# Optimization experiments

Hardware: AMD Instinct MI355X
Metric: run time of the kernel (lower is better)

Reference implementation:

```python
import jax, jax.numpy as jnp
import numpy as np


def setup_inputs() -> dict:
    key = jax.random.key(0)
    kq, kk, kv, km = jax.random.split(key, 4)
    B, H, S, D = 2, 16, 2048, 64
    Q = jax.random.normal(kq, (B, H, S, D), dtype=jnp.float32)
    K = jax.random.normal(kk, (B, H, S, D), dtype=jnp.float32)
    V = jax.random.normal(kv, (B, H, S, D), dtype=jnp.float32)
    mask = jax.random.randint(km, (B, 1, S, S), 0, 2).astype(jnp.bool_)
    return {"Q": Q, "K": K, "V": V, "mask": mask}


def reference(Q, K, V, mask):
    # scores: [B, H, Sq, Sk]
    scores = jnp.einsum("bhqd,bhkd->bhqk", Q, K)
    neg = jnp.finfo(scores.dtype).min
    # Faithful to original: mask fill happens BEFORE the sqrt(d) scaling.
    scores = jnp.where(mask, neg, scores)
    inv_sqrt_d = 1.0 / jnp.sqrt(jnp.asarray(Q.shape[-1], dtype=scores.dtype))
    attn = jax.nn.softmax(scores * inv_sqrt_d, axis=-1)
    return jnp.einsum("bhqk,bhkd->bhqd", attn, V)
```

## Files before the change

### kernel.cpp

```cpp
#include <hip/hip_runtime.h>
#include <stdint.h>


#define SQ 2048
#define DH 64

using bf16x8  = __attribute__((ext_vector_type(8)))  __bf16;
using f32x4   = __attribute__((ext_vector_type(4)))  float;
using ushort8 = __attribute__((ext_vector_type(8)))  unsigned short;
using ushort4v= __attribute__((ext_vector_type(4)))  unsigned short;

static __device__ __forceinline__ unsigned short f2bf(float f) {
    union { float f; uint32_t u; } c; c.f = f;
    return (unsigned short)((c.u + 0x8000u) >> 16);
}

static __device__ __forceinline__ uint32_t pkbf(float a, float b) {
    union { __bf16 h[2]; uint32_t u; } t;
    t.h[0] = (__bf16)a; t.h[1] = (__bf16)b;
    return t.u;
}

static __device__ __forceinline__ f32x4 mfma16(bf16x8 a, bf16x8 b, f32x4 c) {
    return __builtin_amdgcn_mfma_f32_16x16x32_bf16(a, b, c, 0, 0, 0);
}

static __device__ __forceinline__ void gload16(const void* g, void* l) {
    __builtin_amdgcn_global_load_lds(
        (const __attribute__((address_space(1))) void*)g,
        (__attribute__((address_space(3))) void*)l, 16, 0, 0);
}

__global__ __launch_bounds__(256)
void prep_kernel(const int* __restrict__ mask, const float* __restrict__ K,
                 const float* __restrict__ V, unsigned long long* __restrict__ words,
                 unsigned short* __restrict__ Kb, unsigned short* __restrict__ Vt) {
    __shared__ unsigned short tl[64][66];
    const int bx  = blockIdx.x;
    const int tid = threadIdx.x;
    if (bx < 32768) {
        int gid = bx * 256 + tid;
        int mv = mask[gid];
        unsigned long long b = __ballot(mv != 0);
        if ((gid & 63) == 0) words[gid >> 6] = b;
    } else if (bx < 36864) {
        int gid = (bx - 32768) * 256 + tid;
        float4 v = ((const float4*)K)[gid];
        ushort4v t;
        t[0]=f2bf(v.x); t[1]=f2bf(v.y); t[2]=f2bf(v.z); t[3]=f2bf(v.w);
        ((ushort4v*)Kb)[gid] = t;
    } else {
        const int vbx = bx - 36864;
        const int kt  = vbx & 31;
        const size_t bh = vbx >> 5;
        const float* vp = V + (bh * SQ + (size_t)kt * 64) * DH;
        #pragma unroll
        for (int i = 0; i < 4; ++i) {
            int idx = tid + 256 * i;
            int key = idx >> 4;
            int dc  = (idx & 15) * 4;
            float4 v = *(const float4*)(vp + (size_t)key * DH + dc);
            tl[key][dc + 0] = f2bf(v.x);
            tl[key][dc + 1] = f2bf(v.y);
            tl[key][dc + 2] = f2bf(v.z);
            tl[key][dc + 3] = f2bf(v.w);
        }
        __syncthreads();
        unsigned short* op = Vt + bh * DH * SQ + (size_t)kt * 64;
        #pragma unroll
        for (int i = 0; i < 4; ++i) {
            int idx = tid + 256 * i;
            int d  = idx >> 4;
            int kc = (idx & 15) * 4;
            ushort4v t;
            t[0] = tl[kc + 0][d]; t[1] = tl[kc + 1][d];
            t[2] = tl[kc + 2][d]; t[3] = tl[kc + 3][d];
            *(ushort4v*)(op + (size_t)d * SQ + kc) = t;
        }
    }
}

__global__ __launch_bounds__(128, 2)
void attn_kernel(const float* __restrict__ Q,
                 const unsigned short* __restrict__ Kb,
                 const unsigned short* __restrict__ Vtg,
                 const unsigned long long* __restrict__ Mw,
                 float* __restrict__ out) {
    __shared__ __align__(16) unsigned short Ks[2][64 * 64];
    __shared__ __align__(16) unsigned short Vs[2][64 * 64];
    __shared__ __align__(16) unsigned short Ps[2 * 16 * 64];

    const int tid  = threadIdx.x;
    const int w    = tid >> 6;
    const int l    = tid & 63;
    const int quad = l >> 4;
    const int c16  = l & 15;
    const int bx = blockIdx.x;
    const int hh = bx & 15;
    const int b  = (bx >> 4) & 1;
    const int qt = bx >> 5;

    const size_t bh = (size_t)b * 16 + hh;
    const float* Qp = Q + bh * SQ * DH;
    const int qw = qt * 64 + 32 * w;

    const unsigned long long* Mrow0 = Mw + ((size_t)b * SQ + qw + c16) * (SQ / 64);
    const unsigned long long* Mrow1 = Mrow0 + 16 * (SQ / 64);

    const int lr = l >> 3;
    const int gg = l & 7;
    const int off16 = ((gg ^ lr) << 4);
    const char* Kg = (const char*)(Kb  + bh * (size_t)SQ * DH);
    const char* Vg = (const char*)(Vtg + bh * (size_t)DH * SQ);
    const char* kS[4]; const char* vS[4];
    #pragma unroll
    for (int i = 0; i < 4; ++i) {
        int row = 32 * w + 8 * i + lr;
        kS[i] = Kg + (size_t)row * 128  + off16;
        vS[i] = Vg + (size_t)row * 4096 + off16;
    }

    bf16x8 qf[2][2];
    #pragma unroll
    for (int sub = 0; sub < 2; ++sub) {
        const float* qr = Qp + (size_t)(qw + 16 * sub + c16) * DH;
        #pragma unroll
        for (int c = 0; c < 2; ++c) {
            int d0 = 32 * c + 8 * quad;
            float4 a  = *(const float4*)(qr + d0);
            float4 b4 = *(const float4*)(qr + d0 + 4);
            ushort8 t;
            t[0]=f2bf(a.x);  t[1]=f2bf(a.y);  t[2]=f2bf(a.z);  t[3]=f2bf(a.w);
            t[4]=f2bf(b4.x); t[5]=f2bf(b4.y); t[6]=f2bf(b4.z); t[7]=f2bf(b4.w);
            qf[sub][c] = __builtin_bit_cast(bf16x8, t);
        }
    }

    f32x4 o0[4], o1[4];
    float lsum0 = 0.f, lsum1 = 0.f;
    #pragma unroll
    for (int i = 0; i < 4; ++i) { o0[i] = (f32x4)(0.f); o1[i] = (f32x4)(0.f); }

    unsigned short* Pw = Ps + w * (16 * 64);
    const int xg = (c16 & 7);
    int gfrag[2];
    #pragma unroll
    for (int c = 0; c < 2; ++c) gfrag[c] = ((4 * c + quad) ^ xg) << 3;
    int poff[4];
    #pragma unroll
    for (int nb = 0; nb < 4; ++nb)
        poff[nb] = c16 * 64 + (((2 * nb + (quad >> 1)) ^ xg) << 3) + 4 * (quad & 1);
    const int paoff0 = c16 * 64 + gfrag[0];
    const int paoff1 = c16 * 64 + gfrag[1];

    unsigned long long mw0 = Mrow0[0], mw1 = Mrow1[0];
    #pragma unroll
    for (int i = 0; i < 4; ++i) {
        gload16(kS[i], &Ks[0][(4 * w + i) * 512]);
        gload16(vS[i], &Vs[0][(4 * w + i) * 512]);
        kS[i] += 8192; vS[i] += 128;
    }
    __syncthreads();

    for (int t = 0; t < 32; ++t) {
        const int cur = t & 1;

        unsigned long long nmw0 = 0, nmw1 = 0;
        if (t < 31) {
            #pragma unroll
            for (int i = 0; i < 4; ++i) {
                gload16(kS[i], &Ks[cur ^ 1][(4 * w + i) * 512]);
                gload16(vS[i], &Vs[cur ^ 1][(4 * w + i) * 512]);
                kS[i] += 8192; vS[i] += 128;
            }
            nmw0 = Mrow0[t + 1];
            nmw1 = Mrow1[t + 1];
        }

        const unsigned short* Kc = Ks[cur];
        const unsigned short* Vc = Vs[cur];

        f32x4 s0[4], s1[4];
        #pragma unroll
        for (int i = 0; i < 4; ++i) { s0[i] = (f32x4)(0.f); s1[i] = (f32x4)(0.f); }
        __builtin_amdgcn_s_setprio(1);
        #pragma unroll
        for (int c = 0; c < 2; ++c) {
            #pragma unroll
            for (int nb = 0; nb < 4; ++nb) {
                bf16x8 kb = __builtin_bit_cast(bf16x8,
                    *(const ushort8*)&Kc[(c16 + 16 * nb) * 64 + gfrag[c]]);
                s0[nb] = mfma16(kb, qf[0][c], s0[nb]);
                s1[nb] = mfma16(kb, qf[1][c], s1[nb]);
            }
        }
        __builtin_amdgcn_s_setprio(0);

        uint32_t pk0[4][2], pk1[4][2];
        {
            const unsigned long long sh = mw0 >> (4 * quad);
            #pragma unroll
            for (int nb = 0; nb < 4; ++nb) {
                float pv[4];
                #pragma unroll
                for (int r = 0; r < 4; ++r) {
                    float e = __builtin_amdgcn_exp2f(fmaf(s0[nb][r], 0.18033688f, -5.7707802f));
                    pv[r] = ((sh >> (16 * nb + r)) & 1ull) ? 0.0f : e;
                    lsum0 += pv[r];
                }
                pk0[nb][0] = pkbf(pv[0], pv[1]);
                pk0[nb][1] = pkbf(pv[2], pv[3]);
            }
            #pragma unroll
            for (int nb = 0; nb < 4; ++nb) {
                uint2 wv; wv.x = pk0[nb][0]; wv.y = pk0[nb][1];
                *(uint2*)&Pw[poff[nb]] = wv;
            }
        }
        {
            const unsigned long long sh = mw1 >> (4 * quad);
            #pragma unroll
            for (int nb = 0; nb < 4; ++nb) {
                float pv[4];
                #pragma unroll
                for (int r = 0; r < 4; ++r) {
                    float e = __builtin_amdgcn_exp2f(fmaf(s1[nb][r], 0.18033688f, -5.7707802f));
                    pv[r] = ((sh >> (16 * nb + r)) & 1ull) ? 0.0f : e;
                    lsum1 += pv[r];
                }
                pk1[nb][0] = pkbf(pv[0], pv[1]);
                pk1[nb][1] = pkbf(pv[2], pv[3]);
            }
        }
        bf16x8 pa0[2], pa1[2];
        pa0[0] = __builtin_bit_cast(bf16x8, *(const ushort8*)&Pw[paoff0]);
        pa0[1] = __builtin_bit_cast(bf16x8, *(const ushort8*)&Pw[paoff1]);
        #pragma unroll
        for (int nb = 0; nb < 4; ++nb) {
            uint2 wv; wv.x = pk1[nb][0]; wv.y = pk1[nb][1];
            *(uint2*)&Pw[poff[nb]] = wv;
        }
        pa1[0] = __builtin_bit_cast(bf16x8, *(const ushort8*)&Pw[paoff0]);
        pa1[1] = __builtin_bit_cast(bf16x8, *(const ushort8*)&Pw[paoff1]);

        __builtin_amdgcn_s_setprio(1);
        #pragma unroll
        for (int c = 0; c < 2; ++c) {
            #pragma unroll
            for (int db = 0; db < 4; ++db) {
                bf16x8 vb = __builtin_bit_cast(bf16x8,
                    *(const ushort8*)&Vc[(c16 + 16 * db) * 64 + gfrag[c]]);
                o0[db] = mfma16(vb, pa0[c], o0[db]);
                o1[db] = mfma16(vb, pa1[c], o1[db]);
            }
        }
        __builtin_amdgcn_s_setprio(0);

        __syncthreads();
        mw0 = nmw0; mw1 = nmw1;
    }

    {
        float v = lsum0;
        v += __shfl_xor(v, 16, 64);
        v += __shfl_xor(v, 32, 64);
        const float rinv = 1.0f / v;
        float* op = out + (bh * SQ + (size_t)(qw + c16)) * DH + 4 * quad;
        #pragma unroll
        for (int db = 0; db < 4; ++db) {
            float4 st;
            st.x = o0[db][0] * rinv; st.y = o0[db][1] * rinv;
            st.z = o0[db][2] * rinv; st.w = o0[db][3] * rinv;
            *(float4*)(op + 16 * db) = st;
        }
    }
    {
        float v = lsum1;
        v += __shfl_xor(v, 16, 64);
        v += __shfl_xor(v, 32, 64);
        const float rinv = 1.0f / v;
        float* op = out + (bh * SQ + (size_t)(qw + 16 + c16)) * DH + 4 * quad;
        #pragma unroll
        for (int db = 0; db < 4; ++db) {
            float4 st;
            st.x = o1[db][0] * rinv; st.y = o1[db][1] * rinv;
            st.z = o1[db][2] * rinv; st.w = o1[db][3] * rinv;
            *(float4*)(op + 16 * db) = st;
        }
    }
}

extern "C" void kernel_launch(void* const* d_in, const int* in_sizes, int n_in,
                              void* d_out, int out_size, void* d_ws, size_t ws_size,
                              hipStream_t stream) {
    const float* Q    = (const float*)d_in[0];
    const float* K    = (const float*)d_in[1];
    const float* V    = (const float*)d_in[2];
    const int*   mask = (const int*)d_in[3];
    float* out = (float*)d_out;

    char* ws = (char*)d_ws;
    unsigned long long* mwords = (unsigned long long*)ws;
    unsigned short* Kb = (unsigned short*)(ws + (1 << 20));
    unsigned short* Vt = (unsigned short*)(ws + (1 << 20) + (8 << 20));

    prep_kernel<<<dim3(37888), dim3(256), 0, stream>>>(mask, K, V, mwords, Kb, Vt);
    attn_kernel<<<dim3(1024), dim3(128), 0, stream>>>(Q, Kb, Vt, mwords, out);
}
```

Baseline: 190.8 us.

## Load K/V fragments straight from global into registers, one wave per block

Removes the shared-memory K/V double buffering and block-wide barriers. Each 64-thread block handles 32 query rows and reads its K and V MFMA fragments directly from global memory into registers, prefetching the next K tile in software. This cuts LDS traffic and synchronisation, but drops the sharing of K/V tiles between waves, so global/L2 traffic grows. It also raises register pressure from holding the fragments.

```diff
diff --git a/kernel.cpp b/kernel.cpp
--- a/kernel.cpp
+++ b/kernel.cpp
@@ -23,12 +23,6 @@
 
 static __device__ __forceinline__ f32x4 mfma16(bf16x8 a, bf16x8 b, f32x4 c) {
     return __builtin_amdgcn_mfma_f32_16x16x32_bf16(a, b, c, 0, 0, 0);
-}
-
-static __device__ __forceinline__ void gload16(const void* g, void* l) {
-    __builtin_amdgcn_global_load_lds(
-        (const __attribute__((address_space(1))) void*)g,
-        (__attribute__((address_space(3))) void*)l, 16, 0, 0);
 }
 
 __global__ __launch_bounds__(256)
@@ -80,45 +74,42 @@
     }
 }
 
-__global__ __launch_bounds__(128, 2)
+#define LOADKB(dst, kt)                                                          \
+    {                                                                            \
+        _Pragma("unroll")                                                        \
+        for (int nb = 0; nb < 4; ++nb) {                                         \
+            _Pragma("unroll")                                                    \
+            for (int c = 0; c < 2; ++c)                                          \
+                dst[nb][c] = __builtin_bit_cast(bf16x8, *(const ushort8*)        \
+                    (kRow + (size_t)(kt) * 8192 + nb * 2048 + c * 64));          \
+        }                                                                        \
+    }
+
+__global__ __launch_bounds__(64)
 void attn_kernel(const float* __restrict__ Q,
                  const unsigned short* __restrict__ Kb,
                  const unsigned short* __restrict__ Vtg,
                  const unsigned long long* __restrict__ Mw,
                  float* __restrict__ out) {
-    __shared__ __align__(16) unsigned short Ks[2][64 * 64];
-    __shared__ __align__(16) unsigned short Vs[2][64 * 64];
-    __shared__ __align__(16) unsigned short Ps[2 * 16 * 64];
-
-    const int tid  = threadIdx.x;
-    const int w    = tid >> 6;
-    const int l    = tid & 63;
+    __shared__ __align__(16) unsigned short Ps[16 * 64];
+
+    const int l    = threadIdx.x;
     const int quad = l >> 4;
     const int c16  = l & 15;
     const int bx = blockIdx.x;
     const int hh = bx & 15;
     const int b  = (bx >> 4) & 1;
-    const int qt = bx >> 5;
+    const int qs = bx >> 5;
 
     const size_t bh = (size_t)b * 16 + hh;
     const float* Qp = Q + bh * SQ * DH;
-    const int qw = qt * 64 + 32 * w;
+    const int qw = qs * 32;
 
     const unsigned long long* Mrow0 = Mw + ((size_t)b * SQ + qw + c16) * (SQ / 64);
     const unsigned long long* Mrow1 = Mrow0 + 16 * (SQ / 64);
 
-    const int lr = l >> 3;
-    const int gg = l & 7;
-    const int off16 = ((gg ^ lr) << 4);
-    const char* Kg = (const char*)(Kb  + bh * (size_t)SQ * DH);
-    const char* Vg = (const char*)(Vtg + bh * (size_t)DH * SQ);
-    const char* kS[4]; const char* vS[4];
-    #pragma unroll
-    for (int i = 0; i < 4; ++i) {
-        int row = 32 * w + 8 * i + lr;
-        kS[i] = Kg + (size_t)row * 128  + off16;
-        vS[i] = Vg + (size_t)row * 4096 + off16;
-    }
+    const char* kRow = (const char*)(Kb  + bh * (size_t)SQ * DH) + c16 * 128  + quad * 16;
+    const char* vRow = (const char*)(Vtg + bh * (size_t)DH * SQ) + c16 * 4096 + quad * 16;
 
     bf16x8 qf[2][2];
     #pragma unroll
@@ -141,7 +132,7 @@
     #pragma unroll
     for (int i = 0; i < 4; ++i) { o0[i] = (f32x4)(0.f); o1[i] = (f32x4)(0.f); }
 
-    unsigned short* Pw = Ps + w * (16 * 64);
+    unsigned short* Pw = Ps;
     const int xg = (c16 & 7);
     int gfrag[2];
     #pragma unroll
@@ -153,32 +144,17 @@
     const int paoff0 = c16 * 64 + gfrag[0];
     const int paoff1 = c16 * 64 + gfrag[1];
 
-    unsigned long long mw0 = Mrow0[0], mw1 = Mrow1[0];
-    #pragma unroll
-    for (int i = 0; i < 4; ++i) {
-        gload16(kS[i], &Ks[0][(4 * w + i) * 512]);
-        gload16(vS[i], &Vs[0][(4 * w + i) * 512]);
-        kS[i] += 8192; vS[i] += 128;
-    }
-    __syncthreads();
-
-    for (int t = 0; t < 32; ++t) {
-        const int cur = t & 1;
-
-        unsigned long long nmw0 = 0, nmw1 = 0;
-        if (t < 31) {
-            #pragma unroll
-            for (int i = 0; i < 4; ++i) {
-                gload16(kS[i], &Ks[cur ^ 1][(4 * w + i) * 512]);
-                gload16(vS[i], &Vs[cur ^ 1][(4 * w + i) * 512]);
-                kS[i] += 8192; vS[i] += 128;
-            }
-            nmw0 = Mrow0[t + 1];
-            nmw1 = Mrow1[t + 1];
-        }
-
-        const unsigned short* Kc = Ks[cur];
-        const unsigned short* Vc = Vs[cur];
+    auto tile = [&](int kt, bf16x8 (&kb)[4][2]) {
+        unsigned long long mw0 = Mrow0[kt], mw1 = Mrow1[kt];
+
+        bf16x8 vb[4][2];
+        #pragma unroll
+        for (int db = 0; db < 4; ++db) {
+            #pragma unroll
+            for (int c = 0; c < 2; ++c)
+                vb[db][c] = __builtin_bit_cast(bf16x8, *(const ushort8*)
+                    (vRow + db * 65536 + (size_t)kt * 128 + c * 64));
+        }
 
         f32x4 s0[4], s1[4];
         #pragma unroll
@@ -188,10 +164,8 @@
         for (int c = 0; c < 2; ++c) {
             #pragma unroll
             for (int nb = 0; nb < 4; ++nb) {
-                bf16x8 kb = __builtin_bit_cast(bf16x8,
-                    *(const ushort8*)&Kc[(c16 + 16 * nb) * 64 + gfrag[c]]);
-                s0[nb] = mfma16(kb, qf[0][c], s0[nb]);
-                s1[nb] = mfma16(kb, qf[1][c], s1[nb]);
+                s0[nb] = mfma16(kb[nb][c], qf[0][c], s0[nb]);
+                s1[nb] = mfma16(kb[nb][c], qf[1][c], s1[nb]);
             }
         }
         __builtin_amdgcn_s_setprio(0);
@@ -248,16 +222,20 @@
         for (int c = 0; c < 2; ++c) {
             #pragma unroll
             for (int db = 0; db < 4; ++db) {
-                bf16x8 vb = __builtin_bit_cast(bf16x8,
-                    *(const ushort8*)&Vc[(c16 + 16 * db) * 64 + gfrag[c]]);
-                o0[db] = mfma16(vb, pa0[c], o0[db]);
-                o1[db] = mfma16(vb, pa1[c], o1[db]);
+                o0[db] = mfma16(vb[db][c], pa0[c], o0[db]);
+                o1[db] = mfma16(vb[db][c], pa1[c], o1[db]);
             }
         }
         __builtin_amdgcn_s_setprio(0);
-
-        __syncthreads();
-        mw0 = nmw0; mw1 = nmw1;
+    };
+
+    bf16x8 kbA[4][2], kbB[4][2];
+    LOADKB(kbA, 0);
+    for (int tt = 0; tt < 32; tt += 2) {
+        LOADKB(kbB, tt + 1);
+        tile(tt, kbA);
+        if (tt + 2 < 32) LOADKB(kbA, tt + 2);
+        tile(tt + 1, kbB);
     }
 
     {
@@ -305,5 +283,5 @@
     unsigned short* Vt = (unsigned short*)(ws + (1 << 20) + (8 << 20));
 
     prep_kernel<<<dim3(37888), dim3(256), 0, stream>>>(mask, K, V, mwords, Kb, Vt);
-    attn_kernel<<<dim3(1024), dim3(128), 0, stream>>>(Q, Kb, Vt, mwords, out);
-}
+    attn_kernel<<<dim3(2048), dim3(64), 0, stream>>>(Q, Kb, Vt, mwords, out);
+}
```

Result: slower. 250.8 us (+31.5%).

## Load V fragments directly into registers and hand-pipeline K staging with waitcnt

Applied to the files above, without the earlier changes.

V tiles are no longer staged through shared memory. Each lane reads its MFMA B-operand fragments straight from global memory into registers, double-buffered across two tiles. The K loop is unrolled by two with explicit vmcnt and lgkmcnt waits, sched barriers and s_barrier calls, so prefetch of the next tiles overlaps compute. This cuts LDS traffic and footprint, which may allow more occupancy, but it adds register pressure and less-coalesced global V reads, and the hand-counted vmcnt values are fragile.

```diff
diff --git a/kernel.cpp b/kernel.cpp
--- a/kernel.cpp
+++ b/kernel.cpp
@@ -87,7 +87,6 @@
                  const unsigned long long* __restrict__ Mw,
                  float* __restrict__ out) {
     __shared__ __align__(16) unsigned short Ks[2][64 * 64];
-    __shared__ __align__(16) unsigned short Vs[2][64 * 64];
     __shared__ __align__(16) unsigned short Ps[2 * 16 * 64];
 
     const int tid  = threadIdx.x;
@@ -111,14 +110,12 @@
     const int gg = l & 7;
     const int off16 = ((gg ^ lr) << 4);
     const char* Kg = (const char*)(Kb  + bh * (size_t)SQ * DH);
-    const char* Vg = (const char*)(Vtg + bh * (size_t)DH * SQ);
-    const char* kS[4]; const char* vS[4];
-    #pragma unroll
-    for (int i = 0; i < 4; ++i) {
-        int row = 32 * w + 8 * i + lr;
-        kS[i] = Kg + (size_t)row * 128  + off16;
-        vS[i] = Vg + (size_t)row * 4096 + off16;
-    }
+    const char* kBase[4];
+    #pragma unroll
+    for (int i = 0; i < 4; ++i)
+        kBase[i] = Kg + (size_t)(32 * w + 8 * i + lr) * 128 + off16;
+
+    const char* vRow = (const char*)(Vtg + bh * (size_t)DH * SQ) + c16 * 4096 + quad * 16;
 
     bf16x8 qf[2][2];
     #pragma unroll
@@ -153,33 +150,22 @@
     const int paoff0 = c16 * 64 + gfrag[0];
     const int paoff1 = c16 * 64 + gfrag[1];
 
-    unsigned long long mw0 = Mrow0[0], mw1 = Mrow1[0];
-    #pragma unroll
-    for (int i = 0; i < 4; ++i) {
-        gload16(kS[i], &Ks[0][(4 * w + i) * 512]);
-        gload16(vS[i], &Vs[0][(4 * w + i) * 512]);
-        kS[i] += 8192; vS[i] += 128;
-    }
-    __syncthreads();
-
-    for (int t = 0; t < 32; ++t) {
-        const int cur = t & 1;
-
-        unsigned long long nmw0 = 0, nmw1 = 0;
-        if (t < 31) {
-            #pragma unroll
-            for (int i = 0; i < 4; ++i) {
-                gload16(kS[i], &Ks[cur ^ 1][(4 * w + i) * 512]);
-                gload16(vS[i], &Vs[cur ^ 1][(4 * w + i) * 512]);
-                kS[i] += 8192; vS[i] += 128;
-            }
-            nmw0 = Mrow0[t + 1];
-            nmw1 = Mrow1[t + 1];
-        }
-
-        const unsigned short* Kc = Ks[cur];
-        const unsigned short* Vc = Vs[cur];
-
+    auto stageK = [&](int buf, int tile) {
+        #pragma unroll
+        for (int i = 0; i < 4; ++i)
+            gload16(kBase[i] + (size_t)tile * 8192, &Ks[buf][(4 * w + i) * 512]);
+    };
+    auto loadV = [&](bf16x8 (&vb)[4][2], int tile) {
+        #pragma unroll
+        for (int db = 0; db < 4; ++db)
+            #pragma unroll
+            for (int c = 0; c < 2; ++c)
+                vb[db][c] = __builtin_bit_cast(bf16x8, *(const ushort8*)
+                    (vRow + db * 65536 + (size_t)tile * 128 + c * 64));
+    };
+
+    auto computeTile = [&](const unsigned short* Kc, const bf16x8 (&vb)[4][2],
+                           unsigned long long mw0, unsigned long long mw1) {
         f32x4 s0[4], s1[4];
         #pragma unroll
         for (int i = 0; i < 4; ++i) { s0[i] = (f32x4)(0.f); s1[i] = (f32x4)(0.f); }
@@ -248,16 +234,49 @@
         for (int c = 0; c < 2; ++c) {
             #pragma unroll
             for (int db = 0; db < 4; ++db) {
-                bf16x8 vb = __builtin_bit_cast(bf16x8,
-                    *(const ushort8*)&Vc[(c16 + 16 * db) * 64 + gfrag[c]]);
-                o0[db] = mfma16(vb, pa0[c], o0[db]);
-                o1[db] = mfma16(vb, pa1[c], o1[db]);
+                o0[db] = mfma16(vb[db][c], pa0[c], o0[db]);
+                o1[db] = mfma16(vb[db][c], pa1[c], o1[db]);
             }
         }
         __builtin_amdgcn_s_setprio(0);
-
-        __syncthreads();
-        mw0 = nmw0; mw1 = nmw1;
+    };
+
+    bf16x8 vA[4][2], vB[4][2];
+    unsigned long long mA0, mA1, mB0, mB1;
+
+    loadV(vA, 0); stageK(0, 0); mA0 = Mrow0[0]; mA1 = Mrow1[0];
+    __builtin_amdgcn_sched_barrier(0);
+    loadV(vB, 1); stageK(1, 1); mB0 = Mrow0[1]; mB1 = Mrow1[1];
+    __builtin_amdgcn_sched_barrier(0);
+
+    #pragma unroll 1
+    for (int tp = 0; tp < 16; ++tp) {
+        const int t0 = 2 * tp;
+
+        asm volatile("s_waitcnt vmcnt(14)" ::: "memory");
+        __builtin_amdgcn_sched_barrier(0);
+        __builtin_amdgcn_s_barrier();
+        computeTile(Ks[0], vA, mA0, mA1);
+        if (tp < 15) {
+            asm volatile("s_waitcnt lgkmcnt(0)" ::: "memory");
+            __builtin_amdgcn_sched_barrier(0);
+            __builtin_amdgcn_s_barrier();
+            loadV(vA, t0 + 2); stageK(0, t0 + 2);
+            mA0 = Mrow0[t0 + 2]; mA1 = Mrow1[t0 + 2];
+        }
+
+        if (tp < 15) asm volatile("s_waitcnt vmcnt(14)" ::: "memory");
+        else         asm volatile("s_waitcnt vmcnt(0)"  ::: "memory");
+        __builtin_amdgcn_sched_barrier(0);
+        __builtin_amdgcn_s_barrier();
+        computeTile(Ks[1], vB, mB0, mB1);
+        if (tp < 15) {
+            asm volatile("s_waitcnt lgkmcnt(0)" ::: "memory");
+            __builtin_amdgcn_sched_barrier(0);
+            __builtin_amdgcn_s_barrier();
+            loadV(vB, t0 + 3); stageK(1, t0 + 3);
+            mB0 = Mrow0[t0 + 3]; mB1 = Mrow1[t0 + 3];
+        }
     }
 
     {
```

After: 210.0 us. 10.1% more time.

## Keep P in registers by permuting V^T key order to match MFMA fragments

Applied to the files above, without the earlier changes.

Stops round-tripping the softmax probabilities through shared memory. The pre-pass now writes V^T with keys permuted within each 64-key tile, so the register layout of the QK^T accumulator output can be fed directly as the B operand of the PV MFMA. This removes LDS writes and reads plus the shared buffer for P. It relies on the permutation matching the MFMA operand layout exactly, and the PV sum stays correct only because keys are reordered consistently in both operands.

```diff
diff --git a/kernel.cpp b/kernel.cpp
--- a/kernel.cpp
+++ b/kernel.cpp
@@ -9,6 +9,7 @@
 using f32x4   = __attribute__((ext_vector_type(4)))  float;
 using ushort8 = __attribute__((ext_vector_type(8)))  unsigned short;
 using ushort4v= __attribute__((ext_vector_type(4)))  unsigned short;
+using u32x4   = __attribute__((ext_vector_type(4)))  unsigned int;
 
 static __device__ __forceinline__ unsigned short f2bf(float f) {
     union { float f; uint32_t u; } c; c.f = f;
@@ -71,11 +72,13 @@
         for (int i = 0; i < 4; ++i) {
             int idx = tid + 256 * i;
             int d  = idx >> 4;
-            int kc = (idx & 15) * 4;
+            int m  = idx & 15;
+            int kc = m * 4;
+            int pos = 32 * (m >> 3) + 8 * (m & 3) + 4 * ((m >> 2) & 1);
             ushort4v t;
             t[0] = tl[kc + 0][d]; t[1] = tl[kc + 1][d];
             t[2] = tl[kc + 2][d]; t[3] = tl[kc + 3][d];
-            *(ushort4v*)(op + (size_t)d * SQ + kc) = t;
+            *(ushort4v*)(op + (size_t)d * SQ + pos) = t;
         }
     }
 }
@@ -88,7 +91,6 @@
                  float* __restrict__ out) {
     __shared__ __align__(16) unsigned short Ks[2][64 * 64];
     __shared__ __align__(16) unsigned short Vs[2][64 * 64];
-    __shared__ __align__(16) unsigned short Ps[2 * 16 * 64];
 
     const int tid  = threadIdx.x;
     const int w    = tid >> 6;
@@ -141,17 +143,10 @@
     #pragma unroll
     for (int i = 0; i < 4; ++i) { o0[i] = (f32x4)(0.f); o1[i] = (f32x4)(0.f); }
 
-    unsigned short* Pw = Ps + w * (16 * 64);
     const int xg = (c16 & 7);
     int gfrag[2];
     #pragma unroll
     for (int c = 0; c < 2; ++c) gfrag[c] = ((4 * c + quad) ^ xg) << 3;
-    int poff[4];
-    #pragma unroll
-    for (int nb = 0; nb < 4; ++nb)
-        poff[nb] = c16 * 64 + (((2 * nb + (quad >> 1)) ^ xg) << 3) + 4 * (quad & 1);
-    const int paoff0 = c16 * 64 + gfrag[0];
-    const int paoff1 = c16 * 64 + gfrag[1];
 
     unsigned long long mw0 = Mrow0[0], mw1 = Mrow1[0];
     #pragma unroll
@@ -211,11 +206,6 @@
                 pk0[nb][0] = pkbf(pv[0], pv[1]);
                 pk0[nb][1] = pkbf(pv[2], pv[3]);
             }
-            #pragma unroll
-            for (int nb = 0; nb < 4; ++nb) {
-                uint2 wv; wv.x = pk0[nb][0]; wv.y = pk0[nb][1];
-                *(uint2*)&Pw[poff[nb]] = wv;
-            }
         }
         {
             const unsigned long long sh = mw1 >> (4 * quad);
@@ -232,16 +222,18 @@
                 pk1[nb][1] = pkbf(pv[2], pv[3]);
             }
         }
+
         bf16x8 pa0[2], pa1[2];
-        pa0[0] = __builtin_bit_cast(bf16x8, *(const ushort8*)&Pw[paoff0]);
-        pa0[1] = __builtin_bit_cast(bf16x8, *(const ushort8*)&Pw[paoff1]);
-        #pragma unroll
-        for (int nb = 0; nb < 4; ++nb) {
-            uint2 wv; wv.x = pk1[nb][0]; wv.y = pk1[nb][1];
-            *(uint2*)&Pw[poff[nb]] = wv;
-        }
-        pa1[0] = __builtin_bit_cast(bf16x8, *(const ushort8*)&Pw[paoff0]);
-        pa1[1] = __builtin_bit_cast(bf16x8, *(const ushort8*)&Pw[paoff1]);
+        #pragma unroll
+        for (int c = 0; c < 2; ++c) {
+            u32x4 t0v, t1v;
+            t0v[0] = pk0[2 * c][0]; t0v[1] = pk0[2 * c][1];
+            t0v[2] = pk0[2 * c + 1][0]; t0v[3] = pk0[2 * c + 1][1];
+            t1v[0] = pk1[2 * c][0]; t1v[1] = pk1[2 * c][1];
+            t1v[2] = pk1[2 * c + 1][0]; t1v[3] = pk1[2 * c + 1][1];
+            pa0[c] = __builtin_bit_cast(bf16x8, t0v);
+            pa1[c] = __builtin_bit_cast(bf16x8, t1v);
+        }
 
         __builtin_amdgcn_s_setprio(1);
         #pragma unroll
```

Measured after the change: 200.7 us. 1.05x slower.
